# Kernel optimization log

Measured on AMD Instinct MI355X. Metric: run time of the kernel, lower is better.

The kernel has to match this reference:

```python
import jax, jax.numpy as jnp
import numpy as np

B, S = 16, 2048
VOCAB, N_KINGS = 32000, 27
D_EMB, D_MODEL = 256, 512
LN_EPS = 1e-5

def setup_inputs() -> dict:
    key = jax.random.key(0)
    ks = jax.random.split(key, 8)
    sequence = jax.random.randint(ks[0], (B, S), 0, VOCAB)
    king_id = jax.random.randint(ks[1], (B, 1), 0, N_KINGS)
    # stacked per-king token embedding tables (replaces dict-dispatched nn.Embedding modules)
    token_tables = jax.random.normal(ks[2], (N_KINGS, VOCAB, D_EMB), dtype=jnp.float32) * 0.02
    # nn.Bilinear(d_embedding, d_embedding, d_model): weight [M, E1, E2], bias [M]
    Wb = jax.random.normal(ks[3], (D_MODEL, D_EMB, D_EMB), dtype=jnp.float32) * (1.0 / np.sqrt(D_EMB))
    bb = jax.random.normal(ks[4], (D_MODEL,), dtype=jnp.float32) * 0.01
    king_table = jax.random.normal(ks[5], (N_KINGS, D_EMB), dtype=jnp.float32) * 0.02
    gamma = jnp.ones((D_MODEL,), dtype=jnp.float32)
    beta = jnp.zeros((D_MODEL,), dtype=jnp.float32)
    return {"sequence": sequence, "king_id": king_id, "token_tables": token_tables,
            "Wb": Wb, "bb": bb, "king_table": king_table, "gamma": gamma, "beta": beta}

def reference(sequence, king_id, token_tables, Wb, bb, king_table, gamma, beta):
    k = king_id[:, 0]                                  # [B]
    # batched dispatch: per-sample king-specific token embedding -> [B, S, E]
    tok = token_tables[k[:, None], sequence]
    kemb = king_table[k]                               # [B, E]
    # Bilinear(tok, kemb_repeated): kemb is constant over s, so contract it first.
    Wk = jnp.einsum('mij,bj->bmi', Wb, kemb)           # [B, M, E]
    x = jnp.einsum('bsi,bmi->bsm', tok, Wk) + bb       # [B, S, M]
    # LayerNorm over d_model
    mean = jnp.mean(x, axis=-1, keepdims=True)
    var = jnp.mean(jnp.square(x - mean), axis=-1, keepdims=True)
    return (x - mean) * jax.lax.rsqrt(var + LN_EPS) * gamma + beta
```

## Files before the change

kernel.cpp:

```cpp
#include <hip/hip_runtime.h>
#include <hip/hip_bf16.h>

#define B 16
#define S 2048
#define VOCAB 32000
#define D_EMB 256
#define D_MODEL 512
#define LN_EPS 1e-5f

using bf16x8 = __attribute__((ext_vector_type(8))) short;
using f32x4  = __attribute__((ext_vector_type(4))) float;

static __device__ __forceinline__ unsigned short f2bf(float f) {
    __hip_bfloat16 h = __float2bfloat16(f);
    return *reinterpret_cast<unsigned short*>(&h);
}

static __device__ __forceinline__ bf16x8 pack8(f32x4 v0, f32x4 v1) {
    union { unsigned short us[8]; bf16x8 v; } pk;
    pk.us[0] = f2bf(v0.x); pk.us[1] = f2bf(v0.y);
    pk.us[2] = f2bf(v0.z); pk.us[3] = f2bf(v0.w);
    pk.us[4] = f2bf(v1.x); pk.us[5] = f2bf(v1.y);
    pk.us[6] = f2bf(v1.z); pk.us[7] = f2bf(v1.w);
    return pk.v;
}

__global__ __launch_bounds__(256) void wk_mfma(
    const float* __restrict__ Wb,
    const float* __restrict__ king_table,
    const int* __restrict__ king_id,
    unsigned short* __restrict__ Wk)
{
    const int t    = threadIdx.x;
    const int lane = t & 63;
    const int wave = t >> 6;
    const int lr   = lane & 15;
    const int kg   = lane >> 4;

    const int kid = king_id[lr];
    const float* kp = king_table + (size_t)kid * D_EMB + kg * 8;
    bf16x8 bemb[8];
#pragma unroll
    for (int step = 0; step < 8; ++step) {
        f32x4 v0 = *(const f32x4*)(kp + step * 32);
        f32x4 v1 = *(const f32x4*)(kp + step * 32 + 4);
        bemb[step] = pack8(v0, v1);
    }

    const int rbase = (blockIdx.x * 4 + wave) * 64;

#pragma unroll
    for (int mf = 0; mf < 4; ++mf) {
        const float* arow = Wb + (size_t)(rbase + mf * 16 + lr) * D_EMB + kg * 8;
        f32x4 acc = {};
#pragma unroll
        for (int step = 0; step < 8; ++step) {
            f32x4 v0 = *(const f32x4*)(arow + step * 32);
            f32x4 v1 = *(const f32x4*)(arow + step * 32 + 4);
            acc = __builtin_amdgcn_mfma_f32_16x16x32_bf16(
                pack8(v0, v1), bemb[step], acc, 0, 0, 0);
        }
        union { unsigned short us[4]; uint2 q; } st;
        st.us[0] = f2bf(acc[0]); st.us[1] = f2bf(acc[1]);
        st.us[2] = f2bf(acc[2]); st.us[3] = f2bf(acc[3]);
        *(uint2*)(Wk + (size_t)lr * (D_MODEL * D_EMB) + rbase + mf * 16 + kg * 4) = st.q;
    }
}

#define TSB 64

__global__ __launch_bounds__(512, 4) void gemm_ln_mfma(
    const int* __restrict__ seq,
    const int* __restrict__ king_id,
    const float* __restrict__ token_tables,
    const unsigned short* __restrict__ Wk,
    const float* __restrict__ bb,
    const float* __restrict__ gamma,
    const float* __restrict__ beta,
    float* __restrict__ out)
{
    __shared__ unsigned short tokL[TSB][264];
    __shared__ float red_sum[8][TSB];
    __shared__ float red_sq[8][TSB];
    __shared__ float stats[2][TSB];

    const int id   = blockIdx.x;
    const int xcd  = id & 7;
    const int k    = id >> 3;
    const int b    = xcd * 2 + (k >> 5);
    const int tile = k & 31;

    const int s0   = tile * TSB;
    const int t    = threadIdx.x;
    const int lane = t & 63;
    const int wave = t >> 6;
    const int lr   = lane & 15;
    const int kg   = lane >> 4;

    const int kb = king_id[b];
    const float* ttab = token_tables + (size_t)kb * VOCAB * D_EMB;

    const int srow = t >> 3;
    const int sck  = (t & 7) * 16;
    const int tokidx = seq[b * S + s0 + srow];
    const float* srcrow = ttab + (size_t)tokidx * D_EMB + sck;

    {
        f32x4 v0 = *(const f32x4*)(srcrow + 0);
        f32x4 v1 = *(const f32x4*)(srcrow + 4);
        f32x4 v2 = *(const f32x4*)(srcrow + 8);
        f32x4 v3 = *(const f32x4*)(srcrow + 12);
        *(bf16x8*)&tokL[srow][sck]     = pack8(v0, v1);
        *(bf16x8*)&tokL[srow][sck + 8] = pack8(v2, v3);
    }
    __syncthreads();

    f32x4 h0 = *(const f32x4*)(srcrow + 128);
    f32x4 h1 = *(const f32x4*)(srcrow + 132);
    f32x4 h2 = *(const f32x4*)(srcrow + 136);
    f32x4 h3 = *(const f32x4*)(srcrow + 140);

    const int m0 = wave * 64;
    const uint4* aptr[4];
    const uint4* bptr[4];
#pragma unroll
    for (int mf = 0; mf < 4; ++mf)
        aptr[mf] = (const uint4*)&tokL[mf * 16 + lr][kg * 8];
#pragma unroll
    for (int nf = 0; nf < 4; ++nf) {
        int col = m0 + nf * 16 + lr;
        bptr[nf] = (const uint4*)(Wk + ((size_t)(b * D_MODEL + col)) * D_EMB + kg * 8);
    }

    f32x4 acc[4][4] = {};

#pragma unroll
    for (int step = 0; step < 4; ++step) {
        bf16x8 af[4], bfr[4];
#pragma unroll
        for (int mf = 0; mf < 4; ++mf) {
            uint4 q = aptr[mf][step * 4];
            af[mf] = __builtin_bit_cast(bf16x8, q);
        }
#pragma unroll
        for (int nf = 0; nf < 4; ++nf) {
            uint4 q = bptr[nf][step * 4];
            bfr[nf] = __builtin_bit_cast(bf16x8, q);
        }
#pragma unroll
        for (int mf = 0; mf < 4; ++mf)
#pragma unroll
            for (int nf = 0; nf < 4; ++nf)
                acc[mf][nf] = __builtin_amdgcn_mfma_f32_16x16x32_bf16(
                    af[mf], bfr[nf], acc[mf][nf], 0, 0, 0);
    }

    *(bf16x8*)&tokL[srow][128 + sck]     = pack8(h0, h1);
    *(bf16x8*)&tokL[srow][128 + sck + 8] = pack8(h2, h3);
    __syncthreads();

#pragma unroll
    for (int step = 4; step < 8; ++step) {
        bf16x8 af[4], bfr[4];
#pragma unroll
        for (int mf = 0; mf < 4; ++mf) {
            uint4 q = aptr[mf][step * 4];
            af[mf] = __builtin_bit_cast(bf16x8, q);
        }
#pragma unroll
        for (int nf = 0; nf < 4; ++nf) {
            uint4 q = bptr[nf][step * 4];
            bfr[nf] = __builtin_bit_cast(bf16x8, q);
        }
#pragma unroll
        for (int mf = 0; mf < 4; ++mf)
#pragma unroll
            for (int nf = 0; nf < 4; ++nf)
                acc[mf][nf] = __builtin_amdgcn_mfma_f32_16x16x32_bf16(
                    af[mf], bfr[nf], acc[mf][nf], 0, 0, 0);
    }

    float bbv[4], gv[4], bv[4];
#pragma unroll
    for (int nf = 0; nf < 4; ++nf) {
        int col = m0 + nf * 16 + lr;
        bbv[nf] = bb[col];
        gv[nf]  = gamma[col];
        bv[nf]  = beta[col];
    }

#pragma unroll
    for (int mf = 0; mf < 4; ++mf) {
#pragma unroll
        for (int r = 0; r < 4; ++r) {
            float sum = 0.0f, sq = 0.0f;
#pragma unroll
            for (int nf = 0; nf < 4; ++nf) {
                float v = acc[mf][nf][r] + bbv[nf];
                acc[mf][nf][r] = v;
                sum += v;
                sq  += v * v;
            }
#pragma unroll
            for (int off = 1; off < 16; off <<= 1) {
                sum += __shfl_xor(sum, off);
                sq  += __shfl_xor(sq, off);
            }
            if (lr == 0) {
                int row = mf * 16 + kg * 4 + r;
                red_sum[wave][row] = sum;
                red_sq[wave][row]  = sq;
            }
        }
    }
    __syncthreads();

    if (t < TSB) {
        float s = 0.0f, q = 0.0f;
#pragma unroll
        for (int w = 0; w < 8; ++w) { s += red_sum[w][t]; q += red_sq[w][t]; }
        float mean = s * (1.0f / D_MODEL);
        float var  = q * (1.0f / D_MODEL) - mean * mean;
        stats[0][t] = mean;
        stats[1][t] = rsqrtf(var + LN_EPS);
    }
    __syncthreads();

#pragma unroll
    for (int mf = 0; mf < 4; ++mf) {
#pragma unroll
        for (int r = 0; r < 4; ++r) {
            int row = mf * 16 + kg * 4 + r;
            float mean = stats[0][row];
            float rstd = stats[1][row];
            float* op = out + ((size_t)b * S + s0 + row) * D_MODEL + m0 + lr;
#pragma unroll
            for (int nf = 0; nf < 4; ++nf)
                op[nf * 16] = (acc[mf][nf][r] - mean) * rstd * gv[nf] + bv[nf];
        }
    }
}

extern "C" void kernel_launch(void* const* d_in, const int* in_sizes, int n_in,
                              void* d_out, int out_size, void* d_ws, size_t ws_size,
                              hipStream_t stream)
{
    const int*   seq          = (const int*)d_in[0];
    const int*   king_id      = (const int*)d_in[1];
    const float* token_tables = (const float*)d_in[2];
    const float* Wb           = (const float*)d_in[3];
    const float* bb           = (const float*)d_in[4];
    const float* king_table   = (const float*)d_in[5];
    const float* gamma        = (const float*)d_in[6];
    const float* beta         = (const float*)d_in[7];
    float* out = (float*)d_out;

    unsigned short* Wk = (unsigned short*)d_ws;

    wk_mfma<<<dim3((D_MODEL * D_EMB) / 256), dim3(256), 0, stream>>>(
        Wb, king_table, king_id, Wk);
    gemm_ln_mfma<<<dim3(S / TSB * B), dim3(512), 0, stream>>>(
        seq, king_id, token_tables, Wk, bb, gamma, beta, out);
}
```

Baseline: 59.34 us.

## Split token tile into two row halves to overlap epilogue with second GEMM

The 64-row token tile is now processed as two 32-row halves: the first half is gathered and multiplied over the full K, then its LayerNorm and stores run while the second half's gather sits in registers. This moves the stage split from the K dimension to the row dimension, so output writes for the first half overlap the work on the second half and the accumulator footprint halves (8 instead of 16 fragments). In exchange the Wk B-fragments are read from global/L2 twice per block, and the reduction and barrier sequence runs twice.

```diff
diff --git a/kernel.cpp b/kernel.cpp
--- a/kernel.cpp
+++ b/kernel.cpp
@@ -68,6 +68,7 @@
 }
 
 #define TSB 64
+#define HROWS 32
 
 __global__ __launch_bounds__(512, 4) void gemm_ln_mfma(
     const int* __restrict__ seq,
@@ -80,15 +81,15 @@
     float* __restrict__ out)
 {
     __shared__ unsigned short tokL[TSB][264];
-    __shared__ float red_sum[8][TSB];
-    __shared__ float red_sq[8][TSB];
-    __shared__ float stats[2][TSB];
+    __shared__ float red_sum[8][HROWS];
+    __shared__ float red_sq[8][HROWS];
+    __shared__ float stats[2][HROWS];
 
     const int id   = blockIdx.x;
     const int xcd  = id & 7;
-    const int k    = id >> 3;
-    const int b    = xcd * 2 + (k >> 5);
-    const int tile = k & 31;
+    const int kk   = id >> 3;
+    const int b    = xcd * 2 + (kk >> 5);
+    const int tile = kk & 31;
 
     const int s0   = tile * TSB;
     const int t    = threadIdx.x;
@@ -100,46 +101,48 @@
     const int kb = king_id[b];
     const float* ttab = token_tables + (size_t)kb * VOCAB * D_EMB;
 
-    const int srow = t >> 3;
-    const int sck  = (t & 7) * 16;
-    const int tokidx = seq[b * S + s0 + srow];
-    const float* srcrow = ttab + (size_t)tokidx * D_EMB + sck;
+    const int srow = t >> 4;
+    const int sck  = (t & 15) * 16;
+    const int tok0 = seq[b * S + s0 + srow];
+    const int tok1 = seq[b * S + s0 + HROWS + srow];
+    const float* src0 = ttab + (size_t)tok0 * D_EMB + sck;
+    const float* src1 = ttab + (size_t)tok1 * D_EMB + sck;
 
     {
-        f32x4 v0 = *(const f32x4*)(srcrow + 0);
-        f32x4 v1 = *(const f32x4*)(srcrow + 4);
-        f32x4 v2 = *(const f32x4*)(srcrow + 8);
-        f32x4 v3 = *(const f32x4*)(srcrow + 12);
+        f32x4 v0 = *(const f32x4*)(src0 + 0);
+        f32x4 v1 = *(const f32x4*)(src0 + 4);
+        f32x4 v2 = *(const f32x4*)(src0 + 8);
+        f32x4 v3 = *(const f32x4*)(src0 + 12);
         *(bf16x8*)&tokL[srow][sck]     = pack8(v0, v1);
         *(bf16x8*)&tokL[srow][sck + 8] = pack8(v2, v3);
     }
     __syncthreads();
 
-    f32x4 h0 = *(const f32x4*)(srcrow + 128);
-    f32x4 h1 = *(const f32x4*)(srcrow + 132);
-    f32x4 h2 = *(const f32x4*)(srcrow + 136);
-    f32x4 h3 = *(const f32x4*)(srcrow + 140);
+    f32x4 h0 = *(const f32x4*)(src1 + 0);
+    f32x4 h1 = *(const f32x4*)(src1 + 4);
+    f32x4 h2 = *(const f32x4*)(src1 + 8);
+    f32x4 h3 = *(const f32x4*)(src1 + 12);
 
     const int m0 = wave * 64;
-    const uint4* aptr[4];
     const uint4* bptr[4];
-#pragma unroll
-    for (int mf = 0; mf < 4; ++mf)
-        aptr[mf] = (const uint4*)&tokL[mf * 16 + lr][kg * 8];
+    float bbv[4], gv[4], bv[4];
 #pragma unroll
     for (int nf = 0; nf < 4; ++nf) {
         int col = m0 + nf * 16 + lr;
         bptr[nf] = (const uint4*)(Wk + ((size_t)(b * D_MODEL + col)) * D_EMB + kg * 8);
-    }
-
-    f32x4 acc[4][4] = {};
-
-#pragma unroll
-    for (int step = 0; step < 4; ++step) {
-        bf16x8 af[4], bfr[4];
-#pragma unroll
-        for (int mf = 0; mf < 4; ++mf) {
-            uint4 q = aptr[mf][step * 4];
+        bbv[nf] = bb[col];
+        gv[nf]  = gamma[col];
+        bv[nf]  = beta[col];
+    }
+
+    f32x4 acc[2][4] = {};
+
+#pragma unroll
+    for (int step = 0; step < 8; ++step) {
+        bf16x8 af[2], bfr[4];
+#pragma unroll
+        for (int mf = 0; mf < 2; ++mf) {
+            uint4 q = *(const uint4*)&tokL[mf * 16 + lr][step * 32 + kg * 8];
             af[mf] = __builtin_bit_cast(bf16x8, q);
         }
 #pragma unroll
@@ -148,49 +151,18 @@
             bfr[nf] = __builtin_bit_cast(bf16x8, q);
         }
 #pragma unroll
-        for (int mf = 0; mf < 4; ++mf)
+        for (int mf = 0; mf < 2; ++mf)
 #pragma unroll
             for (int nf = 0; nf < 4; ++nf)
                 acc[mf][nf] = __builtin_amdgcn_mfma_f32_16x16x32_bf16(
                     af[mf], bfr[nf], acc[mf][nf], 0, 0, 0);
     }
 
-    *(bf16x8*)&tokL[srow][128 + sck]     = pack8(h0, h1);
-    *(bf16x8*)&tokL[srow][128 + sck + 8] = pack8(h2, h3);
-    __syncthreads();
-
-#pragma unroll
-    for (int step = 4; step < 8; ++step) {
-        bf16x8 af[4], bfr[4];
-#pragma unroll
-        for (int mf = 0; mf < 4; ++mf) {
-            uint4 q = aptr[mf][step * 4];
-            af[mf] = __builtin_bit_cast(bf16x8, q);
-        }
-#pragma unroll
-        for (int nf = 0; nf < 4; ++nf) {
-            uint4 q = bptr[nf][step * 4];
-            bfr[nf] = __builtin_bit_cast(bf16x8, q);
-        }
-#pragma unroll
-        for (int mf = 0; mf < 4; ++mf)
-#pragma unroll
-            for (int nf = 0; nf < 4; ++nf)
-                acc[mf][nf] = __builtin_amdgcn_mfma_f32_16x16x32_bf16(
-                    af[mf], bfr[nf], acc[mf][nf], 0, 0, 0);
-    }
-
-    float bbv[4], gv[4], bv[4];
-#pragma unroll
-    for (int nf = 0; nf < 4; ++nf) {
-        int col = m0 + nf * 16 + lr;
-        bbv[nf] = bb[col];
-        gv[nf]  = gamma[col];
-        bv[nf]  = beta[col];
-    }
-
-#pragma unroll
-    for (int mf = 0; mf < 4; ++mf) {
+    *(bf16x8*)&tokL[HROWS + srow][sck]     = pack8(h0, h1);
+    *(bf16x8*)&tokL[HROWS + srow][sck + 8] = pack8(h2, h3);
+
+#pragma unroll
+    for (int mf = 0; mf < 2; ++mf) {
 #pragma unroll
         for (int r = 0; r < 4; ++r) {
             float sum = 0.0f, sq = 0.0f;
@@ -214,8 +186,7 @@
         }
     }
     __syncthreads();
-
-    if (t < TSB) {
+    if (t < HROWS) {
         float s = 0.0f, q = 0.0f;
 #pragma unroll
         for (int w = 0; w < 8; ++w) { s += red_sum[w][t]; q += red_sq[w][t]; }
@@ -225,15 +196,90 @@
         stats[1][t] = rsqrtf(var + LN_EPS);
     }
     __syncthreads();
-
-#pragma unroll
-    for (int mf = 0; mf < 4; ++mf) {
+#pragma unroll
+    for (int mf = 0; mf < 2; ++mf) {
 #pragma unroll
         for (int r = 0; r < 4; ++r) {
             int row = mf * 16 + kg * 4 + r;
             float mean = stats[0][row];
             float rstd = stats[1][row];
             float* op = out + ((size_t)b * S + s0 + row) * D_MODEL + m0 + lr;
+#pragma unroll
+            for (int nf = 0; nf < 4; ++nf)
+                op[nf * 16] = (acc[mf][nf][r] - mean) * rstd * gv[nf] + bv[nf];
+        }
+    }
+
+#pragma unroll
+    for (int mf = 0; mf < 2; ++mf)
+#pragma unroll
+        for (int nf = 0; nf < 4; ++nf)
+            acc[mf][nf] = (f32x4){};
+
+#pragma unroll
+    for (int step = 0; step < 8; ++step) {
+        bf16x8 af[2], bfr[4];
+#pragma unroll
+        for (int mf = 0; mf < 2; ++mf) {
+            uint4 q = *(const uint4*)&tokL[HROWS + mf * 16 + lr][step * 32 + kg * 8];
+            af[mf] = __builtin_bit_cast(bf16x8, q);
+        }
+#pragma unroll
+        for (int nf = 0; nf < 4; ++nf) {
+            uint4 q = bptr[nf][step * 4];
+            bfr[nf] = __builtin_bit_cast(bf16x8, q);
+        }
+#pragma unroll
+        for (int mf = 0; mf < 2; ++mf)
+#pragma unroll
+            for (int nf = 0; nf < 4; ++nf)
+                acc[mf][nf] = __builtin_amdgcn_mfma_f32_16x16x32_bf16(
+                    af[mf], bfr[nf], acc[mf][nf], 0, 0, 0);
+    }
+
+#pragma unroll
+    for (int mf = 0; mf < 2; ++mf) {
+#pragma unroll
+        for (int r = 0; r < 4; ++r) {
+            float sum = 0.0f, sq = 0.0f;
+#pragma unroll
+            for (int nf = 0; nf < 4; ++nf) {
+                float v = acc[mf][nf][r] + bbv[nf];
+                acc[mf][nf][r] = v;
+                sum += v;
+                sq  += v * v;
+            }
+#pragma unroll
+            for (int off = 1; off < 16; off <<= 1) {
+                sum += __shfl_xor(sum, off);
+                sq  += __shfl_xor(sq, off);
+            }
+            if (lr == 0) {
+                int row = mf * 16 + kg * 4 + r;
+                red_sum[wave][row] = sum;
+                red_sq[wave][row]  = sq;
+            }
+        }
+    }
+    __syncthreads();
+    if (t < HROWS) {
+        float s = 0.0f, q = 0.0f;
+#pragma unroll
+        for (int w = 0; w < 8; ++w) { s += red_sum[w][t]; q += red_sq[w][t]; }
+        float mean = s * (1.0f / D_MODEL);
+        float var  = q * (1.0f / D_MODEL) - mean * mean;
+        stats[0][t] = mean;
+        stats[1][t] = rsqrtf(var + LN_EPS);
+    }
+    __syncthreads();
+#pragma unroll
+    for (int mf = 0; mf < 2; ++mf) {
+#pragma unroll
+        for (int r = 0; r < 4; ++r) {
+            int row = mf * 16 + kg * 4 + r;
+            float mean = stats[0][row];
+            float rstd = stats[1][row];
+            float* op = out + ((size_t)b * S + s0 + HROWS + row) * D_MODEL + m0 + lr;
 #pragma unroll
             for (int nf = 0; nf < 4; ++nf)
                 op[nf * 16] = (acc[mf][nf][r] - mean) * rstd * gv[nf] + bv[nf];
```

New measurement: 72.61 us. 22.4% more time.
